# Kernel tuning notes

Measured on AMD Instinct MI355X. Metric: run time of the kernel, lower is better.

## Reference

```python
import jax, jax.numpy as jnp
import numpy as np

EMO = 1024
FEAT = 1024
K = 128  # aggregation_k
H_LIST = (4, 8, 16)
D_LIST = tuple(EMO // h for h in H_LIST)  # (256, 128, 64)
D_SUM = sum(D_LIST)  # 448
H_SUM = sum(H_LIST)  # 28
N = len(H_LIST)      # 3 subspaces
TEMP = float(np.power(D_SUM, 0.5))


def _block_mask(sizes, total):
    m = np.zeros((len(sizes), total), np.float32)
    off = 0
    for i, s in enumerate(sizes):
        m[i, off:off + s] = 1.0
        off += s
    return jnp.asarray(m)

M_Q_BLK = _block_mask(D_LIST, D_SUM)  # [N, d_sum]
M_V_BLK = _block_mask(H_LIST, H_SUM)  # [N, h_sum]


def setup_inputs() -> dict:
    key = jax.random.key(0)
    ks = iter(jax.random.split(key, 32))
    nrm = lambda shape, s=1.0: jax.random.normal(next(ks), shape, jnp.float32) * s
    B, Lt, Lp, Nv = 32, 1024, 512, 256
    return {
        "emo_embedding": nrm((B, Lt, EMO)),
        "phr_feat": nrm((B, Lp, FEAT)),
        "video_feat": nrm((B, Nv, FEAT)),
        "w_v_W": nrm((FEAT, FEAT), FEAT ** -0.5), "w_v_b": nrm((FEAT,), 0.01),
        "agg_a_W": nrm((FEAT, K), FEAT ** -0.5), "agg_a_b": nrm((K,), 0.01),
        "agg_c_W": nrm((FEAT, EMO), FEAT ** -0.5), "agg_c_b": nrm((EMO,), 0.01),
        "ele_W": nrm((2 * EMO, 1), (2 * EMO) ** -0.5), "ele_b": nrm((1,), 0.01),
        "wq_W": nrm((EMO, D_SUM), EMO ** -0.5), "wq_b": nrm((D_SUM,), 0.01),
        "wk_W": nrm((EMO, D_SUM), EMO ** -0.5), "wk_b": nrm((D_SUM,), 0.01),
        "wv_W": nrm((EMO, H_SUM), EMO ** -0.5), "wv_b": nrm((H_SUM,), 0.01),
        "wr_W": nrm((EMO, N), EMO ** -0.5), "wr_b": nrm((N,), 0.01),
    }


def reference(emo_embedding, phr_feat, video_feat,
              w_v_W, w_v_b, agg_a_W, agg_a_b, agg_c_W, agg_c_b,
              ele_W, ele_b, wq_W, wq_b, wk_W, wk_b, wv_W, wv_b, wr_W, wr_b):
    B, Lt, _ = emo_embedding.shape
    Nv = video_feat.shape[1]
    Lp = phr_feat.shape[1]

    # --- feature_aggregation ---
    # AdaptiveAvgPool1d(Nv); Lp % Nv == 0 so it is an exact reshape-mean.
    phr = phr_feat.reshape(B, Nv, Lp // Nv, FEAT).mean(axis=2)
    combine = jnp.concatenate([phr @ w_v_W + w_v_b, video_feat], axis=1)   # [B, 2*Nv, FEAT]
    attn_a = jax.nn.softmax(combine @ agg_a_W + agg_a_b, axis=-1)          # [B, 2*Nv, K]
    agg_feat = jnp.einsum('bmk,bme->bke', attn_a, combine @ agg_c_W + agg_c_b)  # [B, K, EMO]

    # --- element_routing ---
    A_pool = jnp.einsum('ble,bke->blk', emo_embedding, agg_feat).mean(axis=1)   # [B, K]
    route = jnp.einsum('bk,bke->be', A_pool, agg_feat)[:, None, :]              # [B, 1, EMO]
    route = jnp.broadcast_to(route, emo_embedding.shape)
    R_e = jnp.tanh(jnp.concatenate([emo_embedding, route], axis=-1) @ ele_W + ele_b)  # [B, Lt, 1]
    route_emo = R_e * emo_embedding                                              # [B, Lt, EMO]

    # --- subspace_routing ---
    Q = route_emo @ wq_W + wq_b        # [B, Lt, d_sum]
    Kp = agg_feat @ wk_W + wk_b        # [B, K, d_sum]
    V = agg_feat @ wv_W + wv_b         # [B, K, h_sum]
    Rp = agg_feat @ wr_W + wr_b        # [B, K, N]

    # N masked copies of Q (block subspace masks); K/R are plain repeats, V is masked.
    Qm = (Q[:, None] * M_Q_BLK[None, :, None, :]).reshape(B, N * Lt, D_SUM)
    Kf = jnp.tile(Kp, (1, N, 1))                                         # [B, N*K, d_sum]
    Vf = (V[:, None] * M_V_BLK[None, :, None, :]).reshape(B, N * K, H_SUM)
    Rf = jnp.tile(Rp, (1, N, 1))                                         # [B, N*K, N]

    attn = jax.nn.softmax(jnp.einsum('bqd,bkd->bqk', Qm, Kf) / TEMP, axis=-1)  # [B, N*Lt, N*K]
    O = jnp.tanh(attn @ Vf).reshape(B, N, Lt, H_SUM)
    O_R = (attn @ Rf).reshape(B, N, Lt, N)

    # per-subspace head gating of route_emo
    T_list = []
    hoff = 0
    for i in range(N):
        hi, di = H_LIST[i], D_LIST[i]
        ori = route_emo.reshape(B, Lt, hi, di)
        Oi = O[:, i, :, hoff:hoff + hi][..., None]      # [B, Lt, hi, 1]
        T_list.append((ori * Oi).reshape(B, Lt, EMO))
        hoff += hi
    T = jnp.stack(T_list, axis=1)                        # [B, N, Lt, EMO]

    Rdiag = jnp.stack([O_R[:, j, :, j].mean(axis=-1) for j in range(N)], axis=1)  # [B, N]
    gate = jax.nn.softmax(Rdiag, axis=-1)[:, :, None, None]
    return emo_embedding + (gate * T).sum(axis=1)
```

## Files before the change

kernel.cpp:

```cpp
#include <hip/hip_runtime.h>
#include <math.h>

typedef long long i64;
typedef __attribute__((ext_vector_type(8))) short bf16x8;
typedef __attribute__((ext_vector_type(4))) float f32x4;

#define TEMP_ISQ 0.047245559f

__device__ __forceinline__ unsigned short f2b(float x) {
  union { float f; unsigned u; } a; a.f = x;
  return (unsigned short)((a.u + 0x7fffu + ((a.u >> 16) & 1u)) >> 16);
}
__device__ __forceinline__ float b2f(unsigned short b) {
  union { float f; unsigned u; } a; a.u = ((unsigned)b) << 16; return a.f;
}

template<int BIAS, int OUTM, int RS, int BZDIV, int XMODE = 0>
__global__ __launch_bounds__(256)
void gemm_mfma(const unsigned short* __restrict__ Ab, i64 sA,
               const unsigned short* __restrict__ Bb, i64 sB,
               const float* __restrict__ bias,
               void* __restrict__ Ob, i64 sO,
               unsigned short* __restrict__ O2b, i64 sO2,
               int Nn, int Kd, int ldA, int ldB, int ldO,
               const float* __restrict__ rowScale, i64 sRS,
               const float* __restrict__ rsAdd)
{
  __shared__ unsigned short As[2][4096];
  __shared__ unsigned short Bs[2][4096];
  const int tid = threadIdx.x;
  const int w = tid >> 6, lane = tid & 63;

  const int gx = gridDim.x, gy = gridDim.y;
  int nwg = gx * gy * gridDim.z;
  int bid = blockIdx.x + gx * (blockIdx.y + gy * blockIdx.z);
  int L = bid;
  if ((nwg & 7) == 0) L = (bid & 7) * (nwg >> 3) + (bid >> 3);
  const int bx = L % gx;
  int rem = L / gx;
  const int by = rem % gy;
  const int z  = rem / gy;

  const int m0 = by * 128, n0 = bx * 128;
  int zA = (XMODE == 2) ? z / 3 : z;
  const unsigned short* A;
  const unsigned short* B;
  int KdL = Kd;
  if (XMODE == 3) {
    int bb = z / 3, ii = z - bb * 3;
    const int dof_[3] = {0, 256, 384};
    const int kdt_[3] = {256, 128, 64};
    A = Ab + (i64)bb * sA + dof_[ii];
    B = Bb + dof_[ii];
    KdL = kdt_[ii];
  } else if (XMODE == 2) {
    A = Ab + (i64)zA * sA;
    B = Bb + (i64)z * sB;
  } else {
    A = Ab + (i64)z * sA;
    B = Bb + (i64)(BZDIV == 1 ? z : z / BZDIV) * sB;
  }
  const int wr = w >> 1, wc = w & 1;
  const int rS = tid >> 2, sS = tid & 3;
  const int cL = lane & 15, sl = lane >> 4;

  f32x4 acc[4][4];
  #pragma unroll
  for (int i = 0; i < 4; ++i)
    #pragma unroll
    for (int j = 0; j < 4; ++j) acc[i][j] = (f32x4){0.f, 0.f, 0.f, 0.f};

  auto STAGE = [&](int buf, int k0) {
    #pragma unroll
    for (int q = 0; q < 2; ++q) {
      int r = rS + q * 64;
      int sg = sS ^ ((r >> 1) & 3);
      const unsigned short* sa = A + (i64)(m0 + r) * ldA + k0 + sg * 8;
      const unsigned short* sb = B + (i64)(n0 + r) * ldB + k0 + sg * 8;
      __builtin_amdgcn_global_load_lds(
          (__attribute__((address_space(1))) void*)sa,
          (__attribute__((address_space(3))) void*)&As[buf][r * 32 + sS * 8], 16, 0, 0);
      __builtin_amdgcn_global_load_lds(
          (__attribute__((address_space(1))) void*)sb,
          (__attribute__((address_space(3))) void*)&Bs[buf][r * 32 + sS * 8], 16, 0, 0);
    }
  };

  STAGE(0, 0);
  __syncthreads();

  for (int k0 = 0; k0 < KdL; k0 += 32) {
    const int cur = (k0 >> 5) & 1;
    if (k0 + 32 < KdL) STAGE(cur ^ 1, k0 + 32);
    bf16x8 af[4], bfv[4];
    #pragma unroll
    for (int mi = 0; mi < 4; ++mi) {
      int rr = wr * 64 + mi * 16 + cL;
      int ph = sl ^ ((rr >> 1) & 3);
      af[mi] = *(const bf16x8*)&As[cur][rr * 32 + ph * 8];
    }
    #pragma unroll
    for (int ni = 0; ni < 4; ++ni) {
      int rr = wc * 64 + ni * 16 + cL;
      int ph = sl ^ ((rr >> 1) & 3);
      bfv[ni] = *(const bf16x8*)&Bs[cur][rr * 32 + ph * 8];
    }
    #pragma unroll
    for (int mi = 0; mi < 4; ++mi)
      #pragma unroll
      for (int ni = 0; ni < 4; ++ni)
        acc[mi][ni] = __builtin_amdgcn_mfma_f32_16x16x32_bf16(af[mi], bfv[ni], acc[mi][ni], 0, 0, 0);
    __syncthreads();
  }

  const float* bp = (XMODE == 2) ? (bias + (i64)z * 128) : bias;
  #pragma unroll
  for (int mi = 0; mi < 4; ++mi) {
    const int rowb = m0 + wr * 64 + mi * 16 + sl * 4;
    #pragma unroll
    for (int ni = 0; ni < 4; ++ni) {
      const int col = n0 + wc * 64 + ni * 16 + cL;
      if (col < Nn) {
        float bc = (BIAS == 1) ? bp[col] : 0.f;
        #pragma unroll
        for (int rg = 0; rg < 4; ++rg) {
          float v = acc[mi][ni][rg];
          if (RS) v *= tanhf(rowScale[(i64)zA * sRS + rowb + rg] + rsAdd[zA]);
          v += bc;
          if (BIAS == 2) v += bias[rowb + rg];
          i64 oidx = (i64)(rowb + rg) * ldO + col;
          if (OUTM == 0)      ((float*)Ob)[(i64)z * sO + oidx] = v;
          else if (OUTM == 1) ((unsigned short*)Ob)[(i64)z * sO + oidx] = f2b(v);
          else if (OUTM == 3) ((float*)Ob)[(i64)z * sO + oidx] = tanhf(v * (1.f / 3.f));
          else {
            ((float*)Ob)[(i64)z * sO + oidx] = v;
            O2b[(i64)z * sO2 + oidx] = f2b(v);
          }
        }
      }
    }
  }
}

__global__ __launch_bounds__(256)
void emo_pass1(const float* __restrict__ emo, const float* __restrict__ eleW,
               unsigned short* __restrict__ emoB, float* __restrict__ colPart,
               float* __restrict__ dotE) {
  int b = blockIdx.y, lc = blockIdx.x;
  int t = threadIdx.x, lane = t & 63, w = t >> 6;
  float4 w4 = ((const float4*)eleW)[t];
  float4 acc = make_float4(0.f, 0.f, 0.f, 0.f);
  __shared__ float dw[16][4];
  const float4* src = (const float4*)emo + ((i64)b * 1024 + lc * 16) * 256;
  ushort4* dst = (ushort4*)emoB + ((i64)b * 1024 + lc * 16) * 256;
  #pragma unroll 4
  for (int lr = 0; lr < 16; ++lr) {
    float4 v = src[lr * 256 + t];
    acc.x += v.x; acc.y += v.y; acc.z += v.z; acc.w += v.w;
    float d = v.x * w4.x + v.y * w4.y + v.z * w4.z + v.w * w4.w;
    #pragma unroll
    for (int o = 32; o; o >>= 1) d += __shfl_xor(d, o);
    if (!lane) dw[lr][w] = d;
    ushort4 o4; o4.x = f2b(v.x); o4.y = f2b(v.y); o4.z = f2b(v.z); o4.w = f2b(v.w);
    dst[lr * 256 + t] = o4;
  }
  __syncthreads();
  if (t < 16) dotE[(i64)b * 1024 + lc * 16 + t] = dw[t][0] + dw[t][1] + dw[t][2] + dw[t][3];
  ((float4*)colPart)[((i64)b * 64 + lc) * 256 + t] = acc;
}

__global__ void colmean2(const float* __restrict__ colPart, float* __restrict__ emomean) {
  int b = blockIdx.y, e = blockIdx.x * 256 + threadIdx.x;
  float s = 0.f;
  #pragma unroll 8
  for (int lc = 0; lc < 64; ++lc) s += colPart[((i64)b * 64 + lc) * 1024 + e];
  emomean[b * 1024 + e] = s * (1.f / 1024.f);
}

__global__ __launch_bounds__(256)
void transpose_all(const float* __restrict__ w_v_W, const float* __restrict__ agg_a_W,
                   const float* __restrict__ agg_c_W, const float* __restrict__ wq_W,
                   const float* __restrict__ wk_W, const float* __restrict__ wv_W,
                   const float* __restrict__ wr_W,
                   unsigned short* __restrict__ wvT, unsigned short* __restrict__ aaT,
                   unsigned short* __restrict__ acT, unsigned short* __restrict__ wqB,
                   unsigned short* __restrict__ kvrT) {
  int bx = blockIdx.x;
  int t = threadIdx.x;
  if (bx >= 84) {
    i64 li = (((i64)(bx - 84) * 32 + blockIdx.y) * 256 + t) * 4;
    float4 v = *(const float4*)(wq_W + li);
    ushort4 o; o.x = f2b(v.x); o.y = f2b(v.y); o.z = f2b(v.z); o.w = f2b(v.w);
    *(ushort4*)(wqB + li) = o;
    return;
  }
  __shared__ float T[32][33];
  const float* in; unsigned short* out; int N, Npad, s0;
  if (bx < 32)      { in = w_v_W;   out = wvT;                     N = 1024; Npad = 1024; s0 = 0; }
  else if (bx < 36) { in = agg_a_W; out = aaT;                     N = 128;  Npad = 128;  s0 = 32; }
  else if (bx < 68) { in = agg_c_W; out = acT;                     N = 1024; Npad = 1024; s0 = 36; }
  else if (bx < 82) { in = wk_W;    out = kvrT;                    N = 448;  Npad = 448;  s0 = 68; }
  else if (bx < 83) { in = wv_W;    out = kvrT + (i64)448 * 1024;  N = 28;   Npad = 28;   s0 = 82; }
  else              { in = wr_W;    out = kvrT + (i64)476 * 1024;  N = 3;    Npad = 36;   s0 = 83; }
  int n0 = (bx - s0) * 32, k0 = blockIdx.y * 32;
  #pragma unroll
  for (int p = 0; p < 4; ++p) {
    int idx = t + 256 * p; int kk = idx >> 5, nn = idx & 31;
    float v = 0.f;
    if (n0 + nn < N) v = in[(i64)(k0 + kk) * N + (n0 + nn)];
    T[nn][kk] = v;
  }
  __syncthreads();
  #pragma unroll
  for (int p = 0; p < 4; ++p) {
    int idx = t + 256 * p; int nn = idx >> 5, kk = idx & 31;
    if (n0 + nn < Npad) out[(i64)(n0 + nn) * 1024 + (k0 + kk)] = f2b(T[nn][kk]);
  }
}

__global__ void kvr_bias_kernel(const float* wkb, const float* wvb, const float* wrb, float* out) {
  int t = blockIdx.x * 256 + threadIdx.x;
  if (t >= 480) return;
  out[t] = (t < 448) ? wkb[t] : (t < 476) ? wvb[t - 448] : (t < 479) ? wrb[t - 476] : 0.f;
}

__global__ void qb_kernel(const unsigned short* __restrict__ KVR, const float* __restrict__ wq_b,
                          float* __restrict__ qb) {
  int zz = blockIdx.x;
  int bb = zz / 3, ii = zz - bb * 3;
  const int dof_[3] = {0, 256, 384};
  const int kdt_[3] = {256, 128, 64};
  int k = threadIdx.x;
  const unsigned short* kp = KVR + (i64)bb * 61440 + k * 480 + dof_[ii];
  const float* wb = wq_b + dof_[ii];
  float s = 0.f;
  for (int d = 0; d < kdt_[ii]; ++d) s += b2f(kp[d]) * wb[d];
  qb[zz * 128 + k] = s;
}

__global__ void pool_phr(const float* __restrict__ phr, unsigned short* __restrict__ out) {
  i64 idx = (i64)blockIdx.x * 256 + threadIdx.x;
  if (idx >= 2097152) return;
  i64 bm = idx >> 8; int c = (int)(idx & 255);
  i64 b = bm >> 8, m = bm & 255;
  const float4* r0 = (const float4*)(phr + (b * 512 + 2 * m) * 1024) + c;
  const float4* r1 = (const float4*)(phr + (b * 512 + 2 * m + 1) * 1024) + c;
  float4 a = *r0, d = *r1;
  ushort4 o;
  o.x = f2b(0.5f * (a.x + d.x)); o.y = f2b(0.5f * (a.y + d.y));
  o.z = f2b(0.5f * (a.z + d.z)); o.w = f2b(0.5f * (a.w + d.w));
  ((ushort4*)out)[idx] = o;
}

__global__ void vconv(const float* __restrict__ video, unsigned short* __restrict__ combine) {
  i64 idx = (i64)blockIdx.x * 256 + threadIdx.x;
  if (idx >= 2097152) return;
  i64 b = idx >> 16, r = idx & 65535;
  float4 v = ((const float4*)video)[idx];
  ushort4 o;
  o.x = f2b(v.x); o.y = f2b(v.y); o.z = f2b(v.z); o.w = f2b(v.w);
  ((ushort4*)combine)[b * 131072 + 65536 + r] = o;
}

__global__ void vt_fill(const unsigned short* __restrict__ KVR, unsigned short* __restrict__ VT) {
  int b = blockIdx.y;
  int idx = blockIdx.x * 256 + threadIdx.x;
  int n = idx >> 7, k = idx & 127;
  unsigned short v = 0;
  if (n < 28) v = KVR[(i64)b * 61440 + k * 480 + 448 + n];
  VT[((i64)b * 128 + n) * 128 + k] = v;
}

__global__ void softmax_attn_a(const float* __restrict__ logits, unsigned short* __restrict__ outT) {
  int gw = (int)(((i64)blockIdx.x * blockDim.x + threadIdx.x) >> 6);
  int lane = threadIdx.x & 63;
  if (gw >= 32 * 512) return;
  int b = gw >> 9, m = gw & 511;
  const float* p = logits + (i64)gw * 128;
  float x0 = p[lane], x1 = p[lane + 64];
  float mx = fmaxf(x0, x1);
  #pragma unroll
  for (int o = 32; o; o >>= 1) mx = fmaxf(mx, __shfl_xor(mx, o));
  float e0 = expf(x0 - mx), e1 = expf(x1 - mx);
  float s = e0 + e1;
  #pragma unroll
  for (int o = 32; o; o >>= 1) s += __shfl_xor(s, o);
  float inv = 1.f / s;
  unsigned short* o0 = outT + (i64)b * 128 * 512 + m;
  o0[(i64)lane * 512] = f2b(e0 * inv);
  o0[(i64)(lane + 64) * 512] = f2b(e1 * inv);
}

__global__ void softmax_P_bf(const unsigned short* __restrict__ PL, unsigned short* __restrict__ P) {
  i64 gw = ((i64)blockIdx.x * blockDim.x + threadIdx.x) >> 6;
  int lane = threadIdx.x & 63;
  if (gw >= 98304) return;
  const unsigned short* p = PL + gw * 128;
  float x0 = b2f(p[lane]) * TEMP_ISQ, x1 = b2f(p[lane + 64]) * TEMP_ISQ;
  float mx = fmaxf(x0, x1);
  #pragma unroll
  for (int o = 32; o; o >>= 1) mx = fmaxf(mx, __shfl_xor(mx, o));
  float e0 = expf(x0 - mx), e1 = expf(x1 - mx);
  float s = e0 + e1;
  #pragma unroll
  for (int o = 32; o; o >>= 1) s += __shfl_xor(s, o);
  float inv = 1.f / s;
  P[gw * 128 + lane] = f2b(e0 * inv);
  P[gw * 128 + lane + 64] = f2b(e1 * inv);
}

__global__ void apool_kernel(const float* __restrict__ emomean, const float* __restrict__ agg,
                             float* __restrict__ Apool) {
  int gw = (int)(((i64)blockIdx.x * blockDim.x + threadIdx.x) >> 6);
  int lane = threadIdx.x & 63;
  if (gw >= 32 * 128) return;
  int b = gw >> 7, k = gw & 127;
  const float* ag = agg + ((i64)b * 128 + k) * 1024;
  const float* em = emomean + (i64)b * 1024;
  float s = 0.f;
  #pragma unroll
  for (int j = 0; j < 16; ++j) { int e = j * 64 + lane; s += em[e] * ag[e]; }
  #pragma unroll
  for (int o = 32; o; o >>= 1) s += __shfl_down(s, o);
  if (!lane) Apool[gw] = s;
}

__global__ void route_kernel(const float* __restrict__ Apool, const float* __restrict__ agg,
                             float* __restrict__ route) {
  int b = blockIdx.y;
  int e = blockIdx.x * 256 + threadIdx.x;
  __shared__ float Ap[128];
  if (threadIdx.x < 128) Ap[threadIdx.x] = Apool[b * 128 + threadIdx.x];
  __syncthreads();
  const float* ag = agg + (i64)b * 128 * 1024 + e;
  float s = 0.f;
  #pragma unroll 8
  for (int k = 0; k < 128; ++k) s += Ap[k] * ag[(i64)k * 1024];
  route[b * 1024 + e] = s;
}

__global__ void rb_kernel(const float* __restrict__ route, const float* __restrict__ eleW,
                          const float* __restrict__ eleb, float* __restrict__ rb) {
  int b = blockIdx.x, t = threadIdx.x;
  float s = 0.f;
  for (int j = t; j < 1024; j += 256) s += route[b * 1024 + j] * eleW[1024 + j];
  __shared__ float red[256];
  red[t] = s; __syncthreads();
  for (int o = 128; o > 0; o >>= 1) { if (t < o) red[t] += red[t + o]; __syncthreads(); }
  if (t == 0) rb[b] = red[0] + eleb[0];
}

__global__ void pmean1_kernel(const unsigned short* __restrict__ P, float* __restrict__ Ppart) {
  int bi = blockIdx.x, c = blockIdx.y, k = threadIdx.x;
  const unsigned short* p = P + ((i64)bi * 1024 + c * 128) * 128 + k;
  float s = 0.f;
  for (int l = 0; l < 128; ++l) s += b2f(p[(i64)l * 128]);
  Ppart[((i64)bi * 8 + c) * 128 + k] = s;
}

__global__ void pmean2_rdiag(const float* __restrict__ Ppart, const unsigned short* __restrict__ KVR,
                             float* __restrict__ gate) {
  int b = blockIdx.x, t = threadIdx.x;
  __shared__ float red[128];
  __shared__ float rd[3];
  for (int i = 0; i < 3; ++i) {
    float s = 0.f;
    #pragma unroll
    for (int c = 0; c < 8; ++c) s += Ppart[((i64)(b * 3 + i) * 8 + c) * 128 + t];
    float v = s * (1.f / 1024.f) * b2f(KVR[(i64)b * 61440 + t * 480 + 476 + i]);
    red[t] = v; __syncthreads();
    for (int o = 64; o > 0; o >>= 1) { if (t < o) red[t] += red[t + o]; __syncthreads(); }
    if (t == 0) rd[i] = red[0];
    __syncthreads();
  }
  if (t == 0) {
    float m = fmaxf(rd[0], fmaxf(rd[1], rd[2]));
    float e0 = expf(rd[0] - m), e1 = expf(rd[1] - m), e2 = expf(rd[2] - m);
    float inv = 1.f / (e0 + e1 + e2);
    gate[b * 3 + 0] = e0 * inv; gate[b * 3 + 1] = e1 * inv; gate[b * 3 + 2] = e2 * inv;
  }
}

__global__ __launch_bounds__(256)
void final_kernel(const unsigned short* __restrict__ emoB, const float* __restrict__ dotE,
                  const float* __restrict__ rbv, const float* __restrict__ O,
                  const float* __restrict__ gate, float* __restrict__ out) {
  i64 bl = blockIdx.x;
  int b = (int)(bl >> 10), l = (int)(bl & 1023);
  __shared__ float Gg[16];
  int t = threadIdx.x;
  if (t < 16) {
    float g0 = gate[b * 3], g1 = gate[b * 3 + 1], g2 = gate[b * 3 + 2];
    float o0 = O[((i64)(b * 3 + 0) * 1024 + l) * 28 + (t >> 2)];
    float o1 = O[((i64)(b * 3 + 1) * 1024 + l) * 28 + 4 + (t >> 1)];
    float o2 = O[((i64)(b * 3 + 2) * 1024 + l) * 28 + 12 + t];
    Gg[t] = g0 * o0 + g1 * o1 + g2 * o2;
  }
  __syncthreads();
  float re = tanhf(dotE[bl] + rbv[b]);
  ushort4 e4 = ((const ushort4*)(emoB + bl * 1024))[t];
  float g = 1.f + re * Gg[t >> 4];
  ((float4*)(out + bl * 1024))[t] =
      make_float4(b2f(e4.x) * g, b2f(e4.y) * g, b2f(e4.z) * g, b2f(e4.w) * g);
}

extern "C" void kernel_launch(void* const* d_in, const int* in_sizes, int n_in,
                              void* d_out, int out_size, void* d_ws, size_t ws_size,
                              hipStream_t stream) {
  const float* emo     = (const float*)d_in[0];
  const float* phr     = (const float*)d_in[1];
  const float* video   = (const float*)d_in[2];
  const float* w_v_W   = (const float*)d_in[3];
  const float* w_v_b   = (const float*)d_in[4];
  const float* agg_a_W = (const float*)d_in[5];
  const float* agg_a_b = (const float*)d_in[6];
  const float* agg_c_W = (const float*)d_in[7];
  const float* agg_c_b = (const float*)d_in[8];
  const float* ele_W   = (const float*)d_in[9];
  const float* ele_b   = (const float*)d_in[10];
  const float* wq_W    = (const float*)d_in[11];
  const float* wq_b    = (const float*)d_in[12];
  const float* wk_W    = (const float*)d_in[13];
  const float* wk_b    = (const float*)d_in[14];
  const float* wv_W    = (const float*)d_in[15];
  const float* wv_b    = (const float*)d_in[16];
  const float* wr_W    = (const float*)d_in[17];
  const float* wr_b    = (const float*)d_in[18];

  char* ws = (char*)d_ws;
  const i64 oEmoB    = 0;
  const i64 oCombine = 67108864;
  const i64 oPL      = 67108864;
  const i64 oPooled  = 100663296;
  const i64 oLogitsA = 100663296;
  const i64 oAggF    = 100663296;
  const i64 oO       = 100663296;
  const i64 oCT      = 117440512;
  const i64 oW2T     = 117440512;
  const i64 oAttnAT  = 150994944;
  const i64 oAggB    = 155189248;
  const i64 oWvT     = 163577856;
  const i64 oAaT     = 165675008;
  const i64 oAcT     = 165937152;
  const i64 oWqB     = 168034304;
  const i64 oKvrT    = 169082880;
  const i64 oKVR     = 170131456;
  const i64 oVT      = 174063616;
  const i64 oKvrB    = 175112192;
  const i64 oEmomean = 175116288;
  const i64 oColPart = 175247360;
  const i64 oDotE    = 183635968;
  const i64 oApool   = 183767040;
  const i64 oRoute   = 183783424;
  const i64 oRb      = 183914496;
  const i64 oPpart   = 183914752;
  const i64 oGate    = 184307968;

  unsigned short* emoB    = (unsigned short*)(ws + oEmoB);
  unsigned short* combine = (unsigned short*)(ws + oCombine);
  unsigned short* PL      = (unsigned short*)(ws + oPL);
  unsigned short* P       = PL;
  unsigned short* pooled  = (unsigned short*)(ws + oPooled);
  float*          logitsA = (float*)(ws + oLogitsA);
  float*          aggF    = (float*)(ws + oAggF);
  float*          O       = (float*)(ws + oO);
  unsigned short* CT      = (unsigned short*)(ws + oCT);
  unsigned short* W2T     = (unsigned short*)(ws + oW2T);
  unsigned short* attnAT  = (unsigned short*)(ws + oAttnAT);
  unsigned short* aggB    = (unsigned short*)(ws + oAggB);
  unsigned short* wvT     = (unsigned short*)(ws + oWvT);
  unsigned short* aaT     = (unsigned short*)(ws + oAaT);
  unsigned short* acT     = (unsigned short*)(ws + oAcT);
  unsigned short* wqB     = (unsigned short*)(ws + oWqB);
  unsigned short* kvrT    = (unsigned short*)(ws + oKvrT);
  unsigned short* KVR     = (unsigned short*)(ws + oKVR);
  unsigned short* VT      = (unsigned short*)(ws + oVT);
  float*          kvrB    = (float*)(ws + oKvrB);
  float*          emomean = (float*)(ws + oEmomean);
  float*          colPart = (float*)(ws + oColPart);
  float*          dotE    = (float*)(ws + oDotE);
  float*          Apool   = (float*)(ws + oApool);
  float*          route   = (float*)(ws + oRoute);
  float*          qb      = (float*)(ws + oRoute);
  float*          rbv     = (float*)(ws + oRb);
  float*          Ppart   = (float*)(ws + oPpart);
  float*          gate    = (float*)(ws + oGate);

  dim3 blk(256);

  emo_pass1<<<dim3(64, 32), blk, 0, stream>>>(emo, ele_W, emoB, colPart, dotE);

  transpose_all<<<dim3(98, 32), blk, 0, stream>>>(w_v_W, agg_a_W, agg_c_W, wq_W, wk_W, wv_W, wr_W,
                                                  wvT, aaT, acT, wqB, kvrT);
  kvr_bias_kernel<<<2, blk, 0, stream>>>(wk_b, wv_b, wr_b, kvrB);

  pool_phr<<<8192, blk, 0, stream>>>(phr, pooled);
  vconv<<<8192, blk, 0, stream>>>(video, combine);
  gemm_mfma<1, 1, 0, 1><<<dim3(8, 2, 32), blk, 0, stream>>>(pooled, 262144, wvT, 0, w_v_b,
      (void*)combine, 524288, nullptr, 0, 1024, 1024, 1024, 1024, 1024, nullptr, 0, nullptr);
  gemm_mfma<1, 0, 0, 1><<<dim3(1, 4, 32), blk, 0, stream>>>(combine, 524288, aaT, 0, agg_a_b,
      (void*)logitsA, 65536, nullptr, 0, 128, 1024, 1024, 1024, 128, nullptr, 0, nullptr);
  softmax_attn_a<<<4096, blk, 0, stream>>>(logitsA, attnAT);
  gemm_mfma<2, 1, 0, 1><<<dim3(4, 8, 32), blk, 0, stream>>>(acT, 0, combine, 524288, agg_c_b,
      (void*)CT, 524288, nullptr, 0, 512, 1024, 1024, 1024, 512, nullptr, 0, nullptr);
  gemm_mfma<0, 2, 0, 1><<<dim3(8, 1, 32), blk, 0, stream>>>(attnAT, 65536, CT, 524288, nullptr,
      (void*)aggF, 131072, aggB, 131072, 1024, 512, 512, 512, 1024, nullptr, 0, nullptr);

  colmean2<<<dim3(4, 32), blk, 0, stream>>>(colPart, emomean);
  apool_kernel<<<1024, blk, 0, stream>>>(emomean, aggF, Apool);
  route_kernel<<<dim3(4, 32), blk, 0, stream>>>(Apool, aggF, route);
  rb_kernel<<<32, blk, 0, stream>>>(route, ele_W, ele_b, rbv);

  gemm_mfma<1, 1, 0, 1><<<dim3(4, 1, 32), blk, 0, stream>>>(aggB, 131072, kvrT, 0, kvrB,
      (void*)KVR, 61440, nullptr, 0, 480, 1024, 1024, 1024, 480, nullptr, 0, nullptr);
  vt_fill<<<dim3(64, 32), blk, 0, stream>>>(KVR, VT);

  gemm_mfma<0, 1, 0, 1, 3><<<dim3(8, 1, 96), blk, 0, stream>>>(KVR, 61440, wqB, 0, nullptr,
      (void*)W2T, 131072, nullptr, 0, 1024, 0, 480, 448, 1024, nullptr, 0, nullptr);
  qb_kernel<<<96, 128, 0, stream>>>(KVR, wq_b, qb);

  gemm_mfma<1, 1, 1, 1, 2><<<dim3(1, 8, 96), blk, 0, stream>>>(emoB, 1048576, W2T, 131072, qb,
      (void*)PL, 131072, nullptr, 0, 128, 1024, 1024, 1024, 128, dotE, 1024, rbv);

  softmax_P_bf<<<24576, blk, 0, stream>>>(PL, P);
  pmean1_kernel<<<dim3(96, 8), 128, 0, stream>>>(P, Ppart);
  gemm_mfma<0, 3, 0, 3><<<dim3(1, 8, 96), blk, 0, stream>>>(P, 131072, VT, 16384, nullptr,
      (void*)O, 28672, nullptr, 0, 28, 128, 128, 128, 28, nullptr, 0, nullptr);
  pmean2_rdiag<<<32, 128, 0, stream>>>(Ppart, KVR, gate);
  final_kernel<<<32768, blk, 0, stream>>>(emoB, dotE, rbv, O, gate, (float*)d_out);
}
```

Measured before the change: 453.9 us.

## Fuse softmax into GEMM epilogues and merge small auxiliary kernels

Adds a softmax epilogue to the MFMA GEMM so the attention-logit GEMM and the Q·K GEMM write normalized bf16 probabilities directly (transposed for attn_a). This removes the separate softmax kernels and their logit round-trips through memory. The R column mean is folded into the P@V GEMM as extra columns, which replaces the pmean kernels. Several small elementwise and reduction kernels are merged (pool/video conversion, colmean+apool, route+rb, vt_fill+qb), reducing launch count. The risk is extra shared-memory syncs and exp work in the GEMM epilogue.

```diff
diff --git a/kernel.cpp b/kernel.cpp
--- a/kernel.cpp
+++ b/kernel.cpp
@@ -15,7 +15,7 @@
   union { float f; unsigned u; } a; a.u = ((unsigned)b) << 16; return a.f;
 }
 
-template<int BIAS, int OUTM, int RS, int BZDIV, int XMODE = 0>
+template<int BIAS, int OUTM, int RS, int BZDIV, int XMODE = 0, int SMEPI = 0>
 __global__ __launch_bounds__(256)
 void gemm_mfma(const unsigned short* __restrict__ Ab, i64 sA,
                const unsigned short* __restrict__ Bb, i64 sB,
@@ -114,27 +114,90 @@
   }
 
   const float* bp = (XMODE == 2) ? (bias + (i64)z * 128) : bias;
-  #pragma unroll
-  for (int mi = 0; mi < 4; ++mi) {
-    const int rowb = m0 + wr * 64 + mi * 16 + sl * 4;
-    #pragma unroll
-    for (int ni = 0; ni < 4; ++ni) {
-      const int col = n0 + wc * 64 + ni * 16 + cL;
-      if (col < Nn) {
-        float bc = (BIAS == 1) ? bp[col] : 0.f;
+
+  if constexpr (SMEPI != 0) {
+    const float scale = (SMEPI == 1) ? TEMP_ISQ : 1.f;
+    #pragma unroll
+    for (int mi = 0; mi < 4; ++mi)
+      #pragma unroll
+      for (int ni = 0; ni < 4; ++ni)
         #pragma unroll
         for (int rg = 0; rg < 4; ++rg) {
           float v = acc[mi][ni][rg];
-          if (RS) v *= tanhf(rowScale[(i64)zA * sRS + rowb + rg] + rsAdd[zA]);
-          v += bc;
-          if (BIAS == 2) v += bias[rowb + rg];
-          i64 oidx = (i64)(rowb + rg) * ldO + col;
-          if (OUTM == 0)      ((float*)Ob)[(i64)z * sO + oidx] = v;
-          else if (OUTM == 1) ((unsigned short*)Ob)[(i64)z * sO + oidx] = f2b(v);
-          else if (OUTM == 3) ((float*)Ob)[(i64)z * sO + oidx] = tanhf(v * (1.f / 3.f));
-          else {
-            ((float*)Ob)[(i64)z * sO + oidx] = v;
-            O2b[(i64)z * sO2 + oidx] = f2b(v);
+          if (RS) v *= tanhf(rowScale[(i64)zA * sRS + m0 + wr * 64 + mi * 16 + sl * 4 + rg] + rsAdd[zA]);
+          if (BIAS == 1) v += bp[wc * 64 + ni * 16 + cL];
+          acc[mi][ni][rg] = v * scale;
+        }
+    __shared__ float smax[2][128];
+    __shared__ float ssum[2][128];
+    #pragma unroll
+    for (int mi = 0; mi < 4; ++mi)
+      #pragma unroll
+      for (int rg = 0; rg < 4; ++rg) {
+        float m = fmaxf(fmaxf(acc[mi][0][rg], acc[mi][1][rg]),
+                        fmaxf(acc[mi][2][rg], acc[mi][3][rg]));
+        #pragma unroll
+        for (int o = 1; o < 16; o <<= 1) m = fmaxf(m, __shfl_xor(m, o));
+        if (cL == 0) smax[wc][wr * 64 + mi * 16 + sl * 4 + rg] = m;
+      }
+    __syncthreads();
+    #pragma unroll
+    for (int mi = 0; mi < 4; ++mi)
+      #pragma unroll
+      for (int rg = 0; rg < 4; ++rg) {
+        int r = wr * 64 + mi * 16 + sl * 4 + rg;
+        float m = fmaxf(smax[0][r], smax[1][r]);
+        float s = 0.f;
+        #pragma unroll
+        for (int ni = 0; ni < 4; ++ni) s += expf(acc[mi][ni][rg] - m);
+        #pragma unroll
+        for (int o = 1; o < 16; o <<= 1) s += __shfl_xor(s, o);
+        if (cL == 0) ssum[wc][r] = s;
+      }
+    __syncthreads();
+    unsigned short* OP = (unsigned short*)Ob + (i64)z * sO;
+    #pragma unroll
+    for (int mi = 0; mi < 4; ++mi)
+      #pragma unroll
+      for (int rg = 0; rg < 4; ++rg) {
+        int r = wr * 64 + mi * 16 + sl * 4 + rg;
+        float m = fmaxf(smax[0][r], smax[1][r]);
+        float inv = 1.f / (ssum[0][r] + ssum[1][r]);
+        #pragma unroll
+        for (int ni = 0; ni < 4; ++ni) {
+          int c = wc * 64 + ni * 16 + cL;
+          unsigned short pv = f2b(expf(acc[mi][ni][rg] - m) * inv);
+          if (SMEPI == 1) OP[(i64)(m0 + r) * ldO + c] = pv;
+          else            OP[(i64)c * ldO + (m0 + r)] = pv;
+        }
+      }
+    return;
+  } else {
+    #pragma unroll
+    for (int mi = 0; mi < 4; ++mi) {
+      const int rowb = m0 + wr * 64 + mi * 16 + sl * 4;
+      #pragma unroll
+      for (int ni = 0; ni < 4; ++ni) {
+        const int col = n0 + wc * 64 + ni * 16 + cL;
+        if (col < Nn) {
+          float bc = (BIAS == 1) ? bp[col] : 0.f;
+          #pragma unroll
+          for (int rg = 0; rg < 4; ++rg) {
+            float v = acc[mi][ni][rg];
+            if (RS) v *= tanhf(rowScale[(i64)zA * sRS + rowb + rg] + rsAdd[zA]);
+            v += bc;
+            if (BIAS == 2) v += bias[rowb + rg];
+            i64 oidx = (i64)(rowb + rg) * ldO + col;
+            if (OUTM == 0)      ((float*)Ob)[(i64)z * sO + oidx] = v;
+            else if (OUTM == 1) ((unsigned short*)Ob)[(i64)z * sO + oidx] = f2b(v);
+            else if (OUTM == 3) ((float*)Ob)[(i64)z * sO + oidx] = tanhf(v * (1.f / 3.f));
+            else if (OUTM == 4) {
+              float ov = (col < 28) ? tanhf(v * (1.f / 3.f)) : v * (1.f / 1024.f);
+              ((float*)Ob)[(i64)z * sO + oidx] = ov;
+            } else {
+              ((float*)Ob)[(i64)z * sO + oidx] = v;
+              O2b[(i64)z * sO2 + oidx] = f2b(v);
+            }
           }
         }
       }
@@ -169,14 +232,6 @@
   ((float4*)colPart)[((i64)b * 64 + lc) * 256 + t] = acc;
 }
 
-__global__ void colmean2(const float* __restrict__ colPart, float* __restrict__ emomean) {
-  int b = blockIdx.y, e = blockIdx.x * 256 + threadIdx.x;
-  float s = 0.f;
-  #pragma unroll 8
-  for (int lc = 0; lc < 64; ++lc) s += colPart[((i64)b * 64 + lc) * 1024 + e];
-  emomean[b * 1024 + e] = s * (1.f / 1024.f);
-}
-
 __global__ __launch_bounds__(256)
 void transpose_all(const float* __restrict__ w_v_W, const float* __restrict__ agg_a_W,
                    const float* __restrict__ agg_c_W, const float* __restrict__ wq_W,
@@ -224,151 +279,110 @@
   out[t] = (t < 448) ? wkb[t] : (t < 476) ? wvb[t - 448] : (t < 479) ? wrb[t - 476] : 0.f;
 }
 
-__global__ void qb_kernel(const unsigned short* __restrict__ KVR, const float* __restrict__ wq_b,
-                          float* __restrict__ qb) {
-  int zz = blockIdx.x;
-  int bb = zz / 3, ii = zz - bb * 3;
-  const int dof_[3] = {0, 256, 384};
-  const int kdt_[3] = {256, 128, 64};
-  int k = threadIdx.x;
-  const unsigned short* kp = KVR + (i64)bb * 61440 + k * 480 + dof_[ii];
-  const float* wb = wq_b + dof_[ii];
-  float s = 0.f;
-  for (int d = 0; d < kdt_[ii]; ++d) s += b2f(kp[d]) * wb[d];
-  qb[zz * 128 + k] = s;
-}
-
-__global__ void pool_phr(const float* __restrict__ phr, unsigned short* __restrict__ out) {
+__global__ void pv_conv(const float* __restrict__ phr, const float* __restrict__ video,
+                        unsigned short* __restrict__ pooled, unsigned short* __restrict__ combine) {
   i64 idx = (i64)blockIdx.x * 256 + threadIdx.x;
-  if (idx >= 2097152) return;
-  i64 bm = idx >> 8; int c = (int)(idx & 255);
-  i64 b = bm >> 8, m = bm & 255;
-  const float4* r0 = (const float4*)(phr + (b * 512 + 2 * m) * 1024) + c;
-  const float4* r1 = (const float4*)(phr + (b * 512 + 2 * m + 1) * 1024) + c;
-  float4 a = *r0, d = *r1;
-  ushort4 o;
-  o.x = f2b(0.5f * (a.x + d.x)); o.y = f2b(0.5f * (a.y + d.y));
-  o.z = f2b(0.5f * (a.z + d.z)); o.w = f2b(0.5f * (a.w + d.w));
-  ((ushort4*)out)[idx] = o;
-}
-
-__global__ void vconv(const float* __restrict__ video, unsigned short* __restrict__ combine) {
-  i64 idx = (i64)blockIdx.x * 256 + threadIdx.x;
-  if (idx >= 2097152) return;
-  i64 b = idx >> 16, r = idx & 65535;
-  float4 v = ((const float4*)video)[idx];
-  ushort4 o;
-  o.x = f2b(v.x); o.y = f2b(v.y); o.z = f2b(v.z); o.w = f2b(v.w);
-  ((ushort4*)combine)[b * 131072 + 65536 + r] = o;
-}
-
-__global__ void vt_fill(const unsigned short* __restrict__ KVR, unsigned short* __restrict__ VT) {
-  int b = blockIdx.y;
-  int idx = blockIdx.x * 256 + threadIdx.x;
-  int n = idx >> 7, k = idx & 127;
-  unsigned short v = 0;
-  if (n < 28) v = KVR[(i64)b * 61440 + k * 480 + 448 + n];
-  VT[((i64)b * 128 + n) * 128 + k] = v;
-}
-
-__global__ void softmax_attn_a(const float* __restrict__ logits, unsigned short* __restrict__ outT) {
-  int gw = (int)(((i64)blockIdx.x * blockDim.x + threadIdx.x) >> 6);
-  int lane = threadIdx.x & 63;
-  if (gw >= 32 * 512) return;
-  int b = gw >> 9, m = gw & 511;
-  const float* p = logits + (i64)gw * 128;
-  float x0 = p[lane], x1 = p[lane + 64];
-  float mx = fmaxf(x0, x1);
-  #pragma unroll
-  for (int o = 32; o; o >>= 1) mx = fmaxf(mx, __shfl_xor(mx, o));
-  float e0 = expf(x0 - mx), e1 = expf(x1 - mx);
-  float s = e0 + e1;
-  #pragma unroll
-  for (int o = 32; o; o >>= 1) s += __shfl_xor(s, o);
-  float inv = 1.f / s;
-  unsigned short* o0 = outT + (i64)b * 128 * 512 + m;
-  o0[(i64)lane * 512] = f2b(e0 * inv);
-  o0[(i64)(lane + 64) * 512] = f2b(e1 * inv);
-}
-
-__global__ void softmax_P_bf(const unsigned short* __restrict__ PL, unsigned short* __restrict__ P) {
-  i64 gw = ((i64)blockIdx.x * blockDim.x + threadIdx.x) >> 6;
-  int lane = threadIdx.x & 63;
-  if (gw >= 98304) return;
-  const unsigned short* p = PL + gw * 128;
-  float x0 = b2f(p[lane]) * TEMP_ISQ, x1 = b2f(p[lane + 64]) * TEMP_ISQ;
-  float mx = fmaxf(x0, x1);
-  #pragma unroll
-  for (int o = 32; o; o >>= 1) mx = fmaxf(mx, __shfl_xor(mx, o));
-  float e0 = expf(x0 - mx), e1 = expf(x1 - mx);
-  float s = e0 + e1;
-  #pragma unroll
-  for (int o = 32; o; o >>= 1) s += __shfl_xor(s, o);
-  float inv = 1.f / s;
-  P[gw * 128 + lane] = f2b(e0 * inv);
-  P[gw * 128 + lane + 64] = f2b(e1 * inv);
-}
-
-__global__ void apool_kernel(const float* __restrict__ emomean, const float* __restrict__ agg,
-                             float* __restrict__ Apool) {
-  int gw = (int)(((i64)blockIdx.x * blockDim.x + threadIdx.x) >> 6);
-  int lane = threadIdx.x & 63;
-  if (gw >= 32 * 128) return;
-  int b = gw >> 7, k = gw & 127;
-  const float* ag = agg + ((i64)b * 128 + k) * 1024;
-  const float* em = emomean + (i64)b * 1024;
-  float s = 0.f;
-  #pragma unroll
-  for (int j = 0; j < 16; ++j) { int e = j * 64 + lane; s += em[e] * ag[e]; }
-  #pragma unroll
-  for (int o = 32; o; o >>= 1) s += __shfl_down(s, o);
-  if (!lane) Apool[gw] = s;
-}
-
-__global__ void route_kernel(const float* __restrict__ Apool, const float* __restrict__ agg,
-                             float* __restrict__ route) {
-  int b = blockIdx.y;
-  int e = blockIdx.x * 256 + threadIdx.x;
+  if (idx < 2097152) {
+    i64 bm = idx >> 8; int c = (int)(idx & 255);
+    i64 b = bm >> 8, m = bm & 255;
+    const float4* r0 = (const float4*)(phr + (b * 512 + 2 * m) * 1024) + c;
+    const float4* r1 = (const float4*)(phr + (b * 512 + 2 * m + 1) * 1024) + c;
+    float4 a = *r0, d = *r1;
+    ushort4 o;
+    o.x = f2b(0.5f * (a.x + d.x)); o.y = f2b(0.5f * (a.y + d.y));
+    o.z = f2b(0.5f * (a.z + d.z)); o.w = f2b(0.5f * (a.w + d.w));
+    ((ushort4*)pooled)[idx] = o;
+  } else {
+    i64 j = idx - 2097152;
+    i64 b = j >> 16, r = j & 65535;
+    float4 v = ((const float4*)video)[j];
+    ushort4 o;
+    o.x = f2b(v.x); o.y = f2b(v.y); o.z = f2b(v.z); o.w = f2b(v.w);
+    ((ushort4*)combine)[b * 131072 + 65536 + r] = o;
+  }
+}
+
+__global__ void vtq_fill(const unsigned short* __restrict__ KVR, const float* __restrict__ wq_b,
+                         unsigned short* __restrict__ VT, float* __restrict__ qb) {
+  int b = blockIdx.y, bx = blockIdx.x, t = threadIdx.x;
+  if (bx < 64) {
+    int idx = bx * 256 + t;
+    int n = idx >> 7, k = idx & 127;
+    unsigned short v = 0;
+    if (n < 28)      v = KVR[(i64)b * 61440 + k * 480 + 448 + n];
+    else if (n < 31) v = KVR[(i64)b * 61440 + k * 480 + 476 + (n - 28)];
+    VT[((i64)b * 128 + n) * 128 + k] = v;
+  } else if (t < 128) {
+    int ii = bx - 64;
+    const int dof_[3] = {0, 256, 384};
+    const int kdt_[3] = {256, 128, 64};
+    const unsigned short* kp = KVR + (i64)b * 61440 + t * 480 + dof_[ii];
+    const float* wb = wq_b + dof_[ii];
+    float s = 0.f;
+    for (int d = 0; d < kdt_[ii]; ++d) s += b2f(kp[d]) * wb[d];
+    qb[(b * 3 + ii) * 128 + t] = s;
+  }
+}
+
+__global__ __launch_bounds__(256)
+void colmean_apool(const float* __restrict__ colPart, const float* __restrict__ aggF,
+                   float* __restrict__ Apool) {
+  int b = blockIdx.x, t = threadIdx.x, lane = t & 63, w = t >> 6;
+  __shared__ float em[1024];
+  float4 s = make_float4(0.f, 0.f, 0.f, 0.f);
+  const float4* cp = (const float4*)colPart + (i64)b * 64 * 256 + t;
+  for (int lc = 0; lc < 64; ++lc) {
+    float4 v = cp[lc * 256];
+    s.x += v.x; s.y += v.y; s.z += v.z; s.w += v.w;
+  }
+  em[t * 4 + 0] = s.x * (1.f / 1024.f); em[t * 4 + 1] = s.y * (1.f / 1024.f);
+  em[t * 4 + 2] = s.z * (1.f / 1024.f); em[t * 4 + 3] = s.w * (1.f / 1024.f);
+  __syncthreads();
+  for (int k = w; k < 128; k += 4) {
+    const float* ag = aggF + ((i64)b * 128 + k) * 1024;
+    float d = 0.f;
+    #pragma unroll
+    for (int j = 0; j < 16; ++j) { int e = j * 64 + lane; d += em[e] * ag[e]; }
+    #pragma unroll
+    for (int o = 32; o; o >>= 1) d += __shfl_down(d, o);
+    if (!lane) Apool[b * 128 + k] = d;
+  }
+}
+
+__global__ __launch_bounds__(256)
+void route_rb(const float* __restrict__ Apool, const float* __restrict__ aggF,
+              const float* __restrict__ eleW, const float* __restrict__ eleb,
+              float* __restrict__ rbv) {
+  int b = blockIdx.x, t = threadIdx.x;
   __shared__ float Ap[128];
-  if (threadIdx.x < 128) Ap[threadIdx.x] = Apool[b * 128 + threadIdx.x];
+  if (t < 128) Ap[t] = Apool[b * 128 + t];
   __syncthreads();
-  const float* ag = agg + (i64)b * 128 * 1024 + e;
-  float s = 0.f;
+  float4 r = make_float4(0.f, 0.f, 0.f, 0.f);
+  const float4* ag = (const float4*)(aggF + (i64)b * 128 * 1024) + t;
   #pragma unroll 8
-  for (int k = 0; k < 128; ++k) s += Ap[k] * ag[(i64)k * 1024];
-  route[b * 1024 + e] = s;
-}
-
-__global__ void rb_kernel(const float* __restrict__ route, const float* __restrict__ eleW,
-                          const float* __restrict__ eleb, float* __restrict__ rb) {
-  int b = blockIdx.x, t = threadIdx.x;
-  float s = 0.f;
-  for (int j = t; j < 1024; j += 256) s += route[b * 1024 + j] * eleW[1024 + j];
+  for (int k = 0; k < 128; ++k) {
+    float a = Ap[k];
+    float4 v = ag[(i64)k * 256];
+    r.x += a * v.x; r.y += a * v.y; r.z += a * v.z; r.w += a * v.w;
+  }
+  float4 w4 = ((const float4*)(eleW + 1024))[t];
+  float d = r.x * w4.x + r.y * w4.y + r.z * w4.z + r.w * w4.w;
   __shared__ float red[256];
-  red[t] = s; __syncthreads();
+  red[t] = d; __syncthreads();
   for (int o = 128; o > 0; o >>= 1) { if (t < o) red[t] += red[t + o]; __syncthreads(); }
-  if (t == 0) rb[b] = red[0] + eleb[0];
-}
-
-__global__ void pmean1_kernel(const unsigned short* __restrict__ P, float* __restrict__ Ppart) {
-  int bi = blockIdx.x, c = blockIdx.y, k = threadIdx.x;
-  const unsigned short* p = P + ((i64)bi * 1024 + c * 128) * 128 + k;
-  float s = 0.f;
-  for (int l = 0; l < 128; ++l) s += b2f(p[(i64)l * 128]);
-  Ppart[((i64)bi * 8 + c) * 128 + k] = s;
-}
-
-__global__ void pmean2_rdiag(const float* __restrict__ Ppart, const unsigned short* __restrict__ KVR,
-                             float* __restrict__ gate) {
+  if (t == 0) rbv[b] = red[0] + eleb[0];
+}
+
+__global__ void gate_kernel(const float* __restrict__ O, float* __restrict__ gate) {
   int b = blockIdx.x, t = threadIdx.x;
   __shared__ float red[128];
   __shared__ float rd[3];
   for (int i = 0; i < 3; ++i) {
+    const float* op = O + ((i64)(b * 3 + i) * 1024) * 32 + 28 + i;
     float s = 0.f;
     #pragma unroll
-    for (int c = 0; c < 8; ++c) s += Ppart[((i64)(b * 3 + i) * 8 + c) * 128 + t];
-    float v = s * (1.f / 1024.f) * b2f(KVR[(i64)b * 61440 + t * 480 + 476 + i]);
-    red[t] = v; __syncthreads();
+    for (int l = t; l < 1024; l += 128) s += op[(i64)l * 32];
+    red[t] = s; __syncthreads();
     for (int o = 64; o > 0; o >>= 1) { if (t < o) red[t] += red[t + o]; __syncthreads(); }
     if (t == 0) rd[i] = red[0];
     __syncthreads();
@@ -391,9 +405,9 @@
   int t = threadIdx.x;
   if (t < 16) {
     float g0 = gate[b * 3], g1 = gate[b * 3 + 1], g2 = gate[b * 3 + 2];
-    float o0 = O[((i64)(b * 3 + 0) * 1024 + l) * 28 + (t >> 2)];
-    float o1 = O[((i64)(b * 3 + 1) * 1024 + l) * 28 + 4 + (t >> 1)];
-    float o2 = O[((i64)(b * 3 + 2) * 1024 + l) * 28 + 12 + t];
+    float o0 = O[((i64)(b * 3 + 0) * 1024 + l) * 32 + (t >> 2)];
+    float o1 = O[((i64)(b * 3 + 1) * 1024 + l) * 32 + 4 + (t >> 1)];
+    float o2 = O[((i64)(b * 3 + 2) * 1024 + l) * 32 + 12 + t];
     Gg[t] = g0 * o0 + g1 * o1 + g2 * o2;
   }
   __syncthreads();
@@ -430,9 +444,8 @@
   char* ws = (char*)d_ws;
   const i64 oEmoB    = 0;
   const i64 oCombine = 67108864;
-  const i64 oPL      = 67108864;
+  const i64 oP       = 67108864;
   const i64 oPooled  = 100663296;
-  const i64 oLogitsA = 100663296;
   const i64 oAggF    = 100663296;
   const i64 oO       = 100663296;
   const i64 oCT      = 117440512;
@@ -447,21 +460,17 @@
   const i64 oKVR     = 170131456;
   const i64 oVT      = 174063616;
   const i64 oKvrB    = 175112192;
-  const i64 oEmomean = 175116288;
   const i64 oColPart = 175247360;
   const i64 oDotE    = 183635968;
   const i64 oApool   = 183767040;
-  const i64 oRoute   = 183783424;
+  const i64 oQb      = 183783424;
   const i64 oRb      = 183914496;
-  const i64 oPpart   = 183914752;
   const i64 oGate    = 184307968;
 
   unsigned short* emoB    = (unsigned short*)(ws + oEmoB);
   unsigned short* combine = (unsigned short*)(ws + oCombine);
-  unsigned short* PL      = (unsigned short*)(ws + oPL);
-  unsigned short* P       = PL;
+  unsigned short* P       = (unsigned short*)(ws + oP);
   unsigned short* pooled  = (unsigned short*)(ws + oPooled);
-  float*          logitsA = (float*)(ws + oLogitsA);
   float*          aggF    = (float*)(ws + oAggF);
   float*          O       = (float*)(ws + oO);
   unsigned short* CT      = (unsigned short*)(ws + oCT);
@@ -476,14 +485,11 @@
   unsigned short* KVR     = (unsigned short*)(ws + oKVR);
   unsigned short* VT      = (unsigned short*)(ws + oVT);
   float*          kvrB    = (float*)(ws + oKvrB);
-  float*          emomean = (float*)(ws + oEmomean);
   float*          colPart = (float*)(ws + oColPart);
   float*          dotE    = (float*)(ws + oDotE);
   float*          Apool   = (float*)(ws + oApool);
-  float*          route   = (float*)(ws + oRoute);
-  float*          qb      = (float*)(ws + oRoute);
+  float*          qb      = (float*)(ws + oQb);
   float*          rbv     = (float*)(ws + oRb);
-  float*          Ppart   = (float*)(ws + oPpart);
   float*          gate    = (float*)(ws + oGate);
 
   dim3 blk(256);
@@ -494,38 +500,32 @@
                                                   wvT, aaT, acT, wqB, kvrT);
   kvr_bias_kernel<<<2, blk, 0, stream>>>(wk_b, wv_b, wr_b, kvrB);
 
-  pool_phr<<<8192, blk, 0, stream>>>(phr, pooled);
-  vconv<<<8192, blk, 0, stream>>>(video, combine);
+  pv_conv<<<16384, blk, 0, stream>>>(phr, video, pooled, combine);
   gemm_mfma<1, 1, 0, 1><<<dim3(8, 2, 32), blk, 0, stream>>>(pooled, 262144, wvT, 0, w_v_b,
       (void*)combine, 524288, nullptr, 0, 1024, 1024, 1024, 1024, 1024, nullptr, 0, nullptr);
-  gemm_mfma<1, 0, 0, 1><<<dim3(1, 4, 32), blk, 0, stream>>>(combine, 524288, aaT, 0, agg_a_b,
-      (void*)logitsA, 65536, nullptr, 0, 128, 1024, 1024, 1024, 128, nullptr, 0, nullptr);
-  softmax_attn_a<<<4096, blk, 0, stream>>>(logitsA, attnAT);
+  gemm_mfma<1, 1, 0, 1, 0, 2><<<dim3(1, 4, 32), blk, 0, stream>>>(combine, 524288, aaT, 0, agg_a_b,
+      (void*)attnAT, 65536, nullptr, 0, 128, 1024, 1024, 1024, 512, nullptr, 0, nullptr);
   gemm_mfma<2, 1, 0, 1><<<dim3(4, 8, 32), blk, 0, stream>>>(acT, 0, combine, 524288, agg_c_b,
       (void*)CT, 524288, nullptr, 0, 512, 1024, 1024, 1024, 512, nullptr, 0, nullptr);
   gemm_mfma<0, 2, 0, 1><<<dim3(8, 1, 32), blk, 0, stream>>>(attnAT, 65536, CT, 524288, nullptr,
       (void*)aggF, 131072, aggB, 131072, 1024, 512, 512, 512, 1024, nullptr, 0, nullptr);
 
-  colmean2<<<dim3(4, 32), blk, 0, stream>>>(colPart, emomean);
-  apool_kernel<<<1024, blk, 0, stream>>>(emomean, aggF, Apool);
-  route_kernel<<<dim3(4, 32), blk, 0, stream>>>(Apool, aggF, route);
-  rb_kernel<<<32, blk, 0, stream>>>(route, ele_W, ele_b, rbv);
+  colmean_apool<<<32, blk, 0, stream>>>(colPart, aggF, Apool);
+  route_rb<<<32, blk, 0, stream>>>(Apool, aggF, ele_W, ele_b, rbv);
 
   gemm_mfma<1, 1, 0, 1><<<dim3(4, 1, 32), blk, 0, stream>>>(aggB, 131072, kvrT, 0, kvrB,
       (void*)KVR, 61440, nullptr, 0, 480, 1024, 1024, 1024, 480, nullptr, 0, nullptr);
-  vt_fill<<<dim3(64, 32), blk, 0, stream>>>(KVR, VT);
+  vtq_fill<<<dim3(67, 32), blk, 0, stream>>>(KVR, wq_b, VT, qb);
 
   gemm_mfma<0, 1, 0, 1, 3><<<dim3(8, 1, 96), blk, 0, stream>>>(KVR, 61440, wqB, 0, nullptr,
       (void*)W2T, 131072, nullptr, 0, 1024, 0, 480, 448, 1024, nullptr, 0, nullptr);
-  qb_kernel<<<96, 128, 0, stream>>>(KVR, wq_b, qb);
-
-  gemm_mfma<1, 1, 1, 1, 2><<<dim3(1, 8, 96), blk, 0, stream>>>(emoB, 1048576, W2T, 131072, qb,
-      (void*)PL, 131072, nullptr, 0, 128, 1024, 1024, 1024, 128, dotE, 1024, rbv);
-
-  softmax_P_bf<<<24576, blk, 0, stream>>>(PL, P);
-  pmean1_kernel<<<dim3(96, 8), 128, 0, stream>>>(P, Ppart);
-  gemm_mfma<0, 3, 0, 3><<<dim3(1, 8, 96), blk, 0, stream>>>(P, 131072, VT, 16384, nullptr,
-      (void*)O, 28672, nullptr, 0, 28, 128, 128, 128, 28, nullptr, 0, nullptr);
-  pmean2_rdiag<<<32, 128, 0, stream>>>(Ppart, KVR, gate);
+
+  gemm_mfma<1, 1, 1, 1, 2, 1><<<dim3(1, 8, 96), blk, 0, stream>>>(emoB, 1048576, W2T, 131072, qb,
+      (void*)P, 131072, nullptr, 0, 128, 1024, 1024, 1024, 128, dotE, 1024, rbv);
+
+  gemm_mfma<0, 4, 0, 3><<<dim3(1, 8, 96), blk, 0, stream>>>(P, 131072, VT, 16384, nullptr,
+      (void*)O, 32768, nullptr, 0, 31, 128, 128, 128, 32, nullptr, 0, nullptr);
+
+  gate_kernel<<<32, 128, 0, stream>>>(O, gate);
   final_kernel<<<32768, blk, 0, stream>>>(emoB, dotE, rbv, O, gate, (float*)d_out);
 }
```

New measurement: 476.9 us. 5.1% more time.
